# Performance work log

Hardware: AMD Instinct MI355X
Metric: run time of the kernel (lower is better)

Reference implementation:

```python
import jax, jax.numpy as jnp
import numpy as np
from jax import lax

N_SAMPLES = 64
POS_PER_BATCH = 16  # round(64 * 0.25)
POS_IOU = 0.5
EXCL_IOU = 0.1
IMG_H = 1024.0
IMG_W = 1024.0
BBOX_STD = jnp.array([0.1, 0.1, 0.2, 0.2], dtype=jnp.float32)
EPS = 1e-7


def _iou_matrix(rois, gts):
    # rois (R,4), gts (G,4) in (y1,x1,y2,x2) -> (R,G)
    y1 = jnp.maximum(rois[:, None, 0], gts[None, :, 0])
    x1 = jnp.maximum(rois[:, None, 1], gts[None, :, 1])
    y2 = jnp.minimum(rois[:, None, 2], gts[None, :, 2])
    x2 = jnp.minimum(rois[:, None, 3], gts[None, :, 3])
    inter = jnp.clip(y2 - y1, 0.0) * jnp.clip(x2 - x1, 0.0)
    area_r = jnp.clip(rois[:, 2] - rois[:, 0], 0.0) * jnp.clip(rois[:, 3] - rois[:, 1], 0.0)
    area_g = jnp.clip(gts[:, 2] - gts[:, 0], 0.0) * jnp.clip(gts[:, 3] - gts[:, 1], 0.0)
    union = area_r[:, None] + area_g[None, :] - inter
    return inter / jnp.maximum(union, EPS)


def _get_offsets(rois, gts):
    rh = jnp.maximum(rois[:, 2] - rois[:, 0], EPS)
    rw = jnp.maximum(rois[:, 3] - rois[:, 1], EPS)
    rcy = rois[:, 0] + 0.5 * rh
    rcx = rois[:, 1] + 0.5 * rw
    gh = jnp.maximum(gts[:, 2] - gts[:, 0], EPS)
    gw = jnp.maximum(gts[:, 3] - gts[:, 1], EPS)
    gcy = gts[:, 0] + 0.5 * gh
    gcx = gts[:, 1] + 0.5 * gw
    return jnp.stack([(gcy - rcy) / rh, (gcx - rcx) / rw,
                      jnp.log(gh / rh), jnp.log(gw / rw)], axis=-1)


def _per_image(roi, gt_bbox_n, gt_label):
    # roi (R,4) normalized; gt_bbox_n (G,4) normalized; gt_label (G,)
    roi_valid = jnp.any(roi != 0, axis=1)
    gt_valid = jnp.any(gt_bbox_n != 0, axis=1)
    ious = _iou_matrix(roi, gt_bbox_n)           # (R,G)
    ious = jnp.where(gt_valid[None, :], ious, -1.0)
    max_iou = ious.max(axis=1)
    idx_max_gt = ious.argmax(axis=1)

    pos = roi_valid & (max_iou >= POS_IOU)
    neg = roi_valid & (max_iou < POS_IOU) & (max_iou >= EXCL_IOU)
    R = roi.shape[0]
    ar = jnp.arange(R)
    # deterministic subsample (lowest index first) in place of tf.random_shuffle
    _, pos_idx = lax.top_k(jnp.where(pos, R - ar, 0), POS_PER_BATCH)
    _, neg_idx = lax.top_k(jnp.where(neg, R - ar, 0), N_SAMPLES)
    n_pos = jnp.minimum(pos.sum(), POS_PER_BATCH)
    n_neg = jnp.minimum(neg.sum(), N_SAMPLES - n_pos)

    slots = jnp.arange(N_SAMPLES)
    is_pos = slots < n_pos
    is_neg = (slots >= n_pos) & (slots < n_pos + n_neg)
    valid = is_pos | is_neg
    pidx = pos_idx[jnp.clip(slots, 0, POS_PER_BATCH - 1)]
    nidx = neg_idx[jnp.clip(slots - n_pos, 0, N_SAMPLES - 1)]
    ridx = jnp.where(is_pos, pidx, jnp.where(is_neg, nidx, 0))

    s_roi_raw = roi[ridx]                        # (64,4)
    gidx = idx_max_gt[ridx]
    s_gt = gt_bbox_n[gidx]
    vf = valid.astype(roi.dtype)[:, None]
    s_roi = s_roi_raw * vf
    s_off = (_get_offsets(s_roi_raw, s_gt) * vf) / BBOX_STD
    s_lab = jnp.where(is_pos, gt_label[gidx], 0).astype(jnp.int32)
    return s_roi, s_off, s_lab


def _forward(normalized_rois, gt_bboxes, gt_labels):
    gt_norm = gt_bboxes / jnp.array([IMG_H, IMG_W, IMG_H, IMG_W], dtype=gt_bboxes.dtype)
    return jax.vmap(_per_image)(normalized_rois, gt_norm, gt_labels)


def setup_inputs() -> dict:
    key = jax.random.key(0)
    k1, k2, k3, k4, k5, k6 = jax.random.split(key, 6)
    B, R, G = 8, 20000, 256
    cy = jax.random.uniform(k1, (B, G)) * IMG_H
    cx = jax.random.uniform(k2, (B, G)) * IMG_W
    sz = jax.random.uniform(k3, (B, G, 2)) * 180.0 + 20.0
    y1 = jnp.clip(cy - 0.5 * sz[..., 0], 0, IMG_H)
    y2 = jnp.clip(cy + 0.5 * sz[..., 0], 0, IMG_H)
    x1 = jnp.clip(cx - 0.5 * sz[..., 1], 0, IMG_W)
    x2 = jnp.clip(cx + 0.5 * sz[..., 1], 0, IMG_W)
    gt_bboxes = jnp.stack([y1, x1, y2, x2], axis=-1).astype(jnp.float32)
    gt_labels = jax.random.randint(k4, (B, G), 1, 81, dtype=jnp.int32)
    gt_norm = gt_bboxes / jnp.array([IMG_H, IMG_W, IMG_H, IMG_W], dtype=jnp.float32)
    # jittered copies of gt boxes guarantee positive RoIs
    jit = jnp.clip(jnp.tile(gt_norm, (1, 4, 1)) + 0.02 * jax.random.normal(k5, (B, 4 * G, 4)), 0.0, 1.0)
    rc = jax.random.uniform(k6, (B, R - 4 * G, 4))
    ry1 = jnp.minimum(rc[..., 0], rc[..., 2]); ry2 = jnp.maximum(rc[..., 0], rc[..., 2])
    rx1 = jnp.minimum(rc[..., 1], rc[..., 3]); rx2 = jnp.maximum(rc[..., 1], rc[..., 3])
    rand_rois = jnp.stack([ry1, rx1, ry2, rx2], axis=-1)
    normalized_rois = jnp.concatenate([jit, rand_rois], axis=1).astype(jnp.float32)
    return {"normalized_rois": normalized_rois, "gt_bboxes": gt_bboxes, "gt_labels": gt_labels}


def reference(normalized_rois, gt_bboxes, gt_labels):
    return _forward(normalized_rois, gt_bboxes, gt_labels)
```

## Files before the change

### kernel.cpp

```cpp
#include <hip/hip_runtime.h>

#pragma clang fp contract(off)

#define GMAX 256

__global__ __launch_bounds__(256) void iou_cls_kernel(
    const float* __restrict__ rois, const float* __restrict__ gts,
    int* __restrict__ cls_out, int R, int G)
{
    const int bi = blockIdx.y;
    const int r  = blockIdx.x * 256 + threadIdx.x;

    __shared__ float gy1[GMAX], gx1[GMAX], gy2[GMAX], gx2[GMAX], gar[GMAX];
    __shared__ int   gval[GMAX];

    const int t = threadIdx.x;
    if (t < G && t < GMAX) {
        const float4 g4 = *reinterpret_cast<const float4*>(gts + ((size_t)bi * G + t) * 4);
        const float s = 1.0f / 1024.0f;
        const float a = g4.x * s, b = g4.y * s, c = g4.z * s, d = g4.w * s;
        gy1[t] = a; gx1[t] = b; gy2[t] = c; gx2[t] = d;
        gval[t] = (a != 0.f) || (b != 0.f) || (c != 0.f) || (d != 0.f);
        gar[t] = fmaxf(c - a, 0.f) * fmaxf(d - b, 0.f);
    }
    __syncthreads();
    if (r >= R) return;

    const float4 rr = *reinterpret_cast<const float4*>(rois + ((size_t)bi * R + r) * 4);
    const bool rv = (rr.x != 0.f) || (rr.y != 0.f) || (rr.z != 0.f) || (rr.w != 0.f);
    const float ar = fmaxf(rr.z - rr.x, 0.f) * fmaxf(rr.w - rr.y, 0.f);

    float best = -1.0f;
    int   bidx = 0;
    #pragma unroll 4
    for (int g = 0; g < G; ++g) {
        const float y1 = fmaxf(rr.x, gy1[g]);
        const float x1 = fmaxf(rr.y, gx1[g]);
        const float y2 = fminf(rr.z, gy2[g]);
        const float x2 = fminf(rr.w, gx2[g]);
        const float inter = fmaxf(y2 - y1, 0.f) * fmaxf(x2 - x1, 0.f);
        const float uni   = (ar + gar[g]) - inter;
        float iou = inter / fmaxf(uni, 1e-7f);
        if (!gval[g]) iou = -1.0f;
        if (iou > best) { best = iou; bidx = g; }
    }

    const int pos = (rv && (best >= 0.5f)) ? 1 : 0;
    const int neg = (rv && (best < 0.5f) && (best >= 0.1f)) ? 1 : 0;
    cls_out[(size_t)bi * R + r] = (bidx & 0xFFFF) | (pos << 16) | (neg << 17);
}

__global__ __launch_bounds__(1024) void select_kernel(
    const float* __restrict__ rois, const float* __restrict__ gts,
    const int* __restrict__ labels, const int* __restrict__ cls,
    float* __restrict__ out, int R, int G, int B)
{
    const int bi  = blockIdx.x;
    const int tid = threadIdx.x;
    const int* clsb = cls + (size_t)bi * R;

    const int seg = (R + 1023) >> 10;
    const int s0 = tid * seg;
    const int s1 = min(R, s0 + seg);

    int pc = 0, nc = 0;
    for (int r = s0; r < s1; ++r) {
        const int c = clsb[r];
        pc += (c >> 16) & 1;
        nc += (c >> 17) & 1;
    }

    __shared__ int sp[1024], sn[1024];
    sp[tid] = pc; sn[tid] = nc;
    __syncthreads();
    for (int off = 1; off < 1024; off <<= 1) {
        const int vp = (tid >= off) ? sp[tid - off] : 0;
        const int vn = (tid >= off) ? sn[tid - off] : 0;
        __syncthreads();
        sp[tid] += vp; sn[tid] += vn;
        __syncthreads();
    }
    const int pbase = sp[tid] - pc;
    const int nbase = sn[tid] - nc;
    const int tot_p = sp[1023];
    const int tot_n = sn[1023];

    __shared__ int plist[16], nlist[64];
    if (tid < 16) plist[tid] = 0;
    if (tid < 64) nlist[tid] = 0;
    __syncthreads();

    if ((pbase < 16 && pc > 0) || (nbase < 64 && nc > 0)) {
        int p = pbase, n = nbase;
        for (int r = s0; r < s1; ++r) {
            const int c = clsb[r];
            if ((c >> 16) & 1) { if (p < 16) plist[p] = r; ++p; }
            if ((c >> 17) & 1) { if (n < 64) nlist[n] = r; ++n; }
        }
    }
    __syncthreads();

    const int n_pos = min(tot_p, 16);
    const int n_neg = min(tot_n, 64 - n_pos);

    if (tid < 64) {
        const int slot = tid;
        const bool isp = slot < n_pos;
        const bool isn = (!isp) && (slot < n_pos + n_neg);
        const int pidx = plist[min(slot, 15)];
        const int nidx = nlist[max(0, min(slot - n_pos, 63))];
        const int ridx = isp ? pidx : (isn ? nidx : 0);

        const float4 rr = *reinterpret_cast<const float4*>(rois + ((size_t)bi * R + ridx) * 4);
        const int gidx = clsb[ridx] & 0xFFFF;
        const float4 g4 = *reinterpret_cast<const float4*>(gts + ((size_t)bi * G + gidx) * 4);
        const float s = 1.0f / 1024.0f;
        const float g0 = g4.x * s, g1 = g4.y * s, g2 = g4.z * s, g3 = g4.w * s;

        const float vf = (isp || isn) ? 1.0f : 0.0f;
        const float eps = 1e-7f;

        const float rh  = fmaxf(rr.z - rr.x, eps);
        const float rw  = fmaxf(rr.w - rr.y, eps);
        const float rcy = rr.x + 0.5f * rh;
        const float rcx = rr.y + 0.5f * rw;
        const float gh  = fmaxf(g2 - g0, eps);
        const float gw  = fmaxf(g3 - g1, eps);
        const float gcy = g0 + 0.5f * gh;
        const float gcx = g1 + 0.5f * gw;

        float o0 = (gcy - rcy) / rh;
        float o1 = (gcx - rcx) / rw;
        float o2 = logf(gh / rh);
        float o3 = logf(gw / rw);
        o0 = (o0 * vf) / 0.1f;
        o1 = (o1 * vf) / 0.1f;
        o2 = (o2 * vf) / 0.2f;
        o3 = (o3 * vf) / 0.2f;

        const int base = bi * 64 + slot;
        float4* out_roi = reinterpret_cast<float4*>(out) + base;
        float4* out_off = reinterpret_cast<float4*>(out + (size_t)B * 256) + base;
        *out_roi = make_float4(rr.x * vf, rr.y * vf, rr.z * vf, rr.w * vf);
        *out_off = make_float4(o0, o1, o2, o3);

        const float lab = isp ? (float)labels[(size_t)bi * G + gidx] : 0.0f;
        out[(size_t)B * 512 + base] = lab;
    }
}

extern "C" void kernel_launch(void* const* d_in, const int* in_sizes, int n_in,
                              void* d_out, int out_size, void* d_ws, size_t ws_size,
                              hipStream_t stream)
{
    const float* rois   = (const float*)d_in[0];
    const float* gts    = (const float*)d_in[1];
    const int*   labels = (const int*)d_in[2];
    float* out = (float*)d_out;

    const int B = out_size / 576;
    const int G = in_sizes[2] / B;
    const int R = in_sizes[0] / (4 * B);

    int* cls = (int*)d_ws;

    dim3 gridA((R + 255) / 256, B);
    iou_cls_kernel<<<gridA, 256, 0, stream>>>(rois, gts, cls, R, G);
    select_kernel<<<B, 1024, 0, stream>>>(rois, gts, labels, cls, out, R, G, B);
}
```

Baseline: 111.2 us.

## Replace per-RoI class words with ballot bitmasks and recompute argmax only for selected slots

The first kernel now tracks only the max IoU, with no argmax. Invalid GTs are replaced by far-away boxes with zero area, which removes the per-iteration validity branch. Each wavefront packs its pos/neg flags into 64-bit ballot masks, cutting workspace writes and the select kernel's serial scan over R. The select kernel scans the popcounts with 512 threads, extracts indices with ffs, and recomputes argmax for only the 64 chosen RoIs, using 8 threads per slot combined with a 64-bit atomicMax key that keeps lowest-index tie-breaking. This adds a redundant IoU pass and assumes NW ≤ 512 and G ≤ 256.

```diff
diff --git a/kernel.cpp b/kernel.cpp
--- a/kernel.cpp
+++ b/kernel.cpp
@@ -3,103 +3,123 @@
 #pragma clang fp contract(off)
 
 #define GMAX 256
-
-__global__ __launch_bounds__(256) void iou_cls_kernel(
+#define K1B 128
+
+__device__ __forceinline__ unsigned int ordf(float f) {
+    unsigned int u = __float_as_uint(f);
+    return (u & 0x80000000u) ? ~u : (u | 0x80000000u);
+}
+
+__global__ __launch_bounds__(K1B) void iou_cls_kernel(
     const float* __restrict__ rois, const float* __restrict__ gts,
-    int* __restrict__ cls_out, int R, int G)
+    unsigned long long* __restrict__ pmask, unsigned long long* __restrict__ nmask,
+    int R, int G, int NW)
 {
     const int bi = blockIdx.y;
-    const int r  = blockIdx.x * 256 + threadIdx.x;
-
-    __shared__ float gy1[GMAX], gx1[GMAX], gy2[GMAX], gx2[GMAX], gar[GMAX];
-    __shared__ int   gval[GMAX];
-
-    const int t = threadIdx.x;
-    if (t < G && t < GMAX) {
+    const int r  = blockIdx.x * K1B + threadIdx.x;
+
+    __shared__ float4 gbox[GMAX];
+    __shared__ float  garea[GMAX];
+
+    for (int t = threadIdx.x; t < G; t += K1B) {
+        const float4 g4 = *reinterpret_cast<const float4*>(gts + ((size_t)bi * G + t) * 4);
+        const float s = 1.0f / 1024.0f;
+        float a = g4.x * s, b = g4.y * s, c = g4.z * s, d = g4.w * s;
+        const bool valid = (a != 0.f) || (b != 0.f) || (c != 0.f) || (d != 0.f);
+        if (!valid) { a = 4.f; b = 4.f; c = 4.f; d = 4.f; }
+        gbox[t]  = make_float4(a, b, c, d);
+        garea[t] = valid ? fmaxf(c - a, 0.f) * fmaxf(d - b, 0.f) : 0.0f;
+    }
+    __syncthreads();
+    if (r >= R) return;
+
+    const float4 rr = *reinterpret_cast<const float4*>(rois + ((size_t)bi * R + r) * 4);
+    const bool rv = (rr.x != 0.f) || (rr.y != 0.f) || (rr.z != 0.f) || (rr.w != 0.f);
+    const float ar = fmaxf(rr.z - rr.x, 0.f) * fmaxf(rr.w - rr.y, 0.f);
+
+    float best = 0.0f;
+    #pragma unroll 4
+    for (int g = 0; g < G; ++g) {
+        const float4 gb = gbox[g];
+        const float y1 = fmaxf(rr.x, gb.x);
+        const float x1 = fmaxf(rr.y, gb.y);
+        const float y2 = fminf(rr.z, gb.z);
+        const float x2 = fminf(rr.w, gb.w);
+        const float inter = fmaxf(y2 - y1, 0.f) * fmaxf(x2 - x1, 0.f);
+        const float uni   = (ar + garea[g]) - inter;
+        const float iou   = inter / fmaxf(uni, 1e-7f);
+        best = fmaxf(best, iou);
+    }
+
+    const bool pos = rv && (best >= 0.5f);
+    const bool neg = rv && !(best >= 0.5f) && (best >= 0.1f);
+
+    const unsigned long long bp = __ballot(pos);
+    const unsigned long long bn = __ballot(neg);
+    const int w = r >> 6;
+    if ((threadIdx.x & 63) == 0 && w < NW) {
+        pmask[(size_t)bi * NW + w] = bp;
+        nmask[(size_t)bi * NW + w] = bn;
+    }
+}
+
+__global__ __launch_bounds__(512) void select_kernel(
+    const float* __restrict__ rois, const float* __restrict__ gts,
+    const int* __restrict__ labels,
+    const unsigned long long* __restrict__ pmask, const unsigned long long* __restrict__ nmask,
+    float* __restrict__ out, int R, int G, int B, int NW)
+{
+    const int bi  = blockIdx.x;
+    const int tid = threadIdx.x;
+
+    __shared__ int sp[512], sn[512];
+    __shared__ float4 sgt[GMAX];
+    __shared__ float  sgv[GMAX];
+    __shared__ int plist[16], nlist[64];
+    __shared__ int sridx[64];
+    __shared__ unsigned long long skey[64];
+
+    for (int t = tid; t < G; t += 512) {
         const float4 g4 = *reinterpret_cast<const float4*>(gts + ((size_t)bi * G + t) * 4);
         const float s = 1.0f / 1024.0f;
         const float a = g4.x * s, b = g4.y * s, c = g4.z * s, d = g4.w * s;
-        gy1[t] = a; gx1[t] = b; gy2[t] = c; gx2[t] = d;
-        gval[t] = (a != 0.f) || (b != 0.f) || (c != 0.f) || (d != 0.f);
-        gar[t] = fmaxf(c - a, 0.f) * fmaxf(d - b, 0.f);
-    }
-    __syncthreads();
-    if (r >= R) return;
-
-    const float4 rr = *reinterpret_cast<const float4*>(rois + ((size_t)bi * R + r) * 4);
-    const bool rv = (rr.x != 0.f) || (rr.y != 0.f) || (rr.z != 0.f) || (rr.w != 0.f);
-    const float ar = fmaxf(rr.z - rr.x, 0.f) * fmaxf(rr.w - rr.y, 0.f);
-
-    float best = -1.0f;
-    int   bidx = 0;
-    #pragma unroll 4
-    for (int g = 0; g < G; ++g) {
-        const float y1 = fmaxf(rr.x, gy1[g]);
-        const float x1 = fmaxf(rr.y, gx1[g]);
-        const float y2 = fminf(rr.z, gy2[g]);
-        const float x2 = fminf(rr.w, gx2[g]);
-        const float inter = fmaxf(y2 - y1, 0.f) * fmaxf(x2 - x1, 0.f);
-        const float uni   = (ar + gar[g]) - inter;
-        float iou = inter / fmaxf(uni, 1e-7f);
-        if (!gval[g]) iou = -1.0f;
-        if (iou > best) { best = iou; bidx = g; }
-    }
-
-    const int pos = (rv && (best >= 0.5f)) ? 1 : 0;
-    const int neg = (rv && (best < 0.5f) && (best >= 0.1f)) ? 1 : 0;
-    cls_out[(size_t)bi * R + r] = (bidx & 0xFFFF) | (pos << 16) | (neg << 17);
-}
-
-__global__ __launch_bounds__(1024) void select_kernel(
-    const float* __restrict__ rois, const float* __restrict__ gts,
-    const int* __restrict__ labels, const int* __restrict__ cls,
-    float* __restrict__ out, int R, int G, int B)
-{
-    const int bi  = blockIdx.x;
-    const int tid = threadIdx.x;
-    const int* clsb = cls + (size_t)bi * R;
-
-    const int seg = (R + 1023) >> 10;
-    const int s0 = tid * seg;
-    const int s1 = min(R, s0 + seg);
-
-    int pc = 0, nc = 0;
-    for (int r = s0; r < s1; ++r) {
-        const int c = clsb[r];
-        pc += (c >> 16) & 1;
-        nc += (c >> 17) & 1;
-    }
-
-    __shared__ int sp[1024], sn[1024];
-    sp[tid] = pc; sn[tid] = nc;
-    __syncthreads();
-    for (int off = 1; off < 1024; off <<= 1) {
+        sgt[t] = make_float4(a, b, c, d);
+        sgv[t] = ((a != 0.f) || (b != 0.f) || (c != 0.f) || (d != 0.f)) ? 1.0f : 0.0f;
+    }
+
+    unsigned long long mp = 0ull, mn = 0ull;
+    if (tid < NW) {
+        mp = pmask[(size_t)bi * NW + tid];
+        mn = nmask[(size_t)bi * NW + tid];
+    }
+    const int cp = __popcll(mp);
+    const int cn = __popcll(mn);
+    sp[tid] = cp; sn[tid] = cn;
+    if (tid < 16) plist[tid] = 0;
+    if (tid < 64) nlist[tid] = 0;
+    __syncthreads();
+    for (int off = 1; off < 512; off <<= 1) {
         const int vp = (tid >= off) ? sp[tid - off] : 0;
         const int vn = (tid >= off) ? sn[tid - off] : 0;
         __syncthreads();
         sp[tid] += vp; sn[tid] += vn;
         __syncthreads();
     }
-    const int pbase = sp[tid] - pc;
-    const int nbase = sn[tid] - nc;
-    const int tot_p = sp[1023];
-    const int tot_n = sn[1023];
-
-    __shared__ int plist[16], nlist[64];
-    if (tid < 16) plist[tid] = 0;
-    if (tid < 64) nlist[tid] = 0;
-    __syncthreads();
-
-    if ((pbase < 16 && pc > 0) || (nbase < 64 && nc > 0)) {
-        int p = pbase, n = nbase;
-        for (int r = s0; r < s1; ++r) {
-            const int c = clsb[r];
-            if ((c >> 16) & 1) { if (p < 16) plist[p] = r; ++p; }
-            if ((c >> 17) & 1) { if (n < 64) nlist[n] = r; ++n; }
-        }
-    }
-    __syncthreads();
-
+    const int basep = sp[tid] - cp;
+    const int basen = sn[tid] - cn;
+
+    if (mp && basep < 16) {
+        int rank = basep; unsigned long long m = mp;
+        while (m && rank < 16) { const int b = __ffsll(m) - 1; plist[rank++] = tid * 64 + b; m &= m - 1; }
+    }
+    if (mn && basen < 64) {
+        int rank = basen; unsigned long long m = mn;
+        while (m && rank < 64) { const int b = __ffsll(m) - 1; nlist[rank++] = tid * 64 + b; m &= m - 1; }
+    }
+    __syncthreads();
+
+    const int tot_p = sp[511];
+    const int tot_n = sn[511];
     const int n_pos = min(tot_p, 16);
     const int n_neg = min(tot_n, 64 - n_pos);
 
@@ -107,16 +127,49 @@
         const int slot = tid;
         const bool isp = slot < n_pos;
         const bool isn = (!isp) && (slot < n_pos + n_neg);
-        const int pidx = plist[min(slot, 15)];
-        const int nidx = nlist[max(0, min(slot - n_pos, 63))];
-        const int ridx = isp ? pidx : (isn ? nidx : 0);
-
+        sridx[slot] = isp ? plist[slot] : (isn ? nlist[slot - n_pos] : 0);
+        skey[slot]  = 0ull;
+    }
+    __syncthreads();
+
+    {
+        const int slot = tid >> 3;
+        const int sub  = tid & 7;
+        const int ridx = sridx[slot];
         const float4 rr = *reinterpret_cast<const float4*>(rois + ((size_t)bi * R + ridx) * 4);
-        const int gidx = clsb[ridx] & 0xFFFF;
-        const float4 g4 = *reinterpret_cast<const float4*>(gts + ((size_t)bi * G + gidx) * 4);
-        const float s = 1.0f / 1024.0f;
-        const float g0 = g4.x * s, g1 = g4.y * s, g2 = g4.z * s, g3 = g4.w * s;
-
+        const float ar = fmaxf(rr.z - rr.x, 0.f) * fmaxf(rr.w - rr.y, 0.f);
+        float best = -1.0f;
+        int bidx = sub * 32;
+        for (int j = 0; j < 32; ++j) {
+            const int g = sub * 32 + j;
+            if (g >= G) break;
+            const float4 gb = sgt[g];
+            const float y1 = fmaxf(rr.x, gb.x);
+            const float x1 = fmaxf(rr.y, gb.y);
+            const float y2 = fminf(rr.z, gb.z);
+            const float x2 = fminf(rr.w, gb.w);
+            const float inter = fmaxf(y2 - y1, 0.f) * fmaxf(x2 - x1, 0.f);
+            const float ga = fmaxf(gb.z - gb.x, 0.f) * fmaxf(gb.w - gb.y, 0.f);
+            const float uni = (ar + ga) - inter;
+            float v = inter / fmaxf(uni, 1e-7f);
+            if (sgv[g] == 0.0f) v = -1.0f;
+            if (v > best) { best = v; bidx = g; }
+        }
+        const unsigned long long key =
+            ((unsigned long long)ordf(best) << 32) | (unsigned int)(~(unsigned int)bidx);
+        atomicMax(&skey[slot], key);
+    }
+    __syncthreads();
+
+    if (tid < 64) {
+        const int slot = tid;
+        const bool isp = slot < n_pos;
+        const bool isn = (!isp) && (slot < n_pos + n_neg);
+        const int ridx = sridx[slot];
+        const int gidx = (int)(~(unsigned int)(skey[slot] & 0xFFFFFFFFull));
+
+        const float4 rr = *reinterpret_cast<const float4*>(rois + ((size_t)bi * R + ridx) * 4);
+        const float4 gb = sgt[gidx];
         const float vf = (isp || isn) ? 1.0f : 0.0f;
         const float eps = 1e-7f;
 
@@ -124,10 +177,10 @@
         const float rw  = fmaxf(rr.w - rr.y, eps);
         const float rcy = rr.x + 0.5f * rh;
         const float rcx = rr.y + 0.5f * rw;
-        const float gh  = fmaxf(g2 - g0, eps);
-        const float gw  = fmaxf(g3 - g1, eps);
-        const float gcy = g0 + 0.5f * gh;
-        const float gcx = g1 + 0.5f * gw;
+        const float gh  = fmaxf(gb.z - gb.x, eps);
+        const float gw  = fmaxf(gb.w - gb.y, eps);
+        const float gcy = gb.x + 0.5f * gh;
+        const float gcx = gb.y + 0.5f * gw;
 
         float o0 = (gcy - rcy) / rh;
         float o1 = (gcx - rcx) / rw;
@@ -139,13 +192,9 @@
         o3 = (o3 * vf) / 0.2f;
 
         const int base = bi * 64 + slot;
-        float4* out_roi = reinterpret_cast<float4*>(out) + base;
-        float4* out_off = reinterpret_cast<float4*>(out + (size_t)B * 256) + base;
-        *out_roi = make_float4(rr.x * vf, rr.y * vf, rr.z * vf, rr.w * vf);
-        *out_off = make_float4(o0, o1, o2, o3);
-
-        const float lab = isp ? (float)labels[(size_t)bi * G + gidx] : 0.0f;
-        out[(size_t)B * 512 + base] = lab;
+        reinterpret_cast<float4*>(out)[base] = make_float4(rr.x * vf, rr.y * vf, rr.z * vf, rr.w * vf);
+        reinterpret_cast<float4*>(out + (size_t)B * 256)[base] = make_float4(o0, o1, o2, o3);
+        out[(size_t)B * 512 + base] = isp ? (float)labels[(size_t)bi * G + gidx] : 0.0f;
     }
 }
 
@@ -161,10 +210,12 @@
     const int B = out_size / 576;
     const int G = in_sizes[2] / B;
     const int R = in_sizes[0] / (4 * B);
-
-    int* cls = (int*)d_ws;
-
-    dim3 gridA((R + 255) / 256, B);
-    iou_cls_kernel<<<gridA, 256, 0, stream>>>(rois, gts, cls, R, G);
-    select_kernel<<<B, 1024, 0, stream>>>(rois, gts, labels, cls, out, R, G, B);
-}
+    const int NW = (R + 63) / 64;
+
+    unsigned long long* pmask = (unsigned long long*)d_ws;
+    unsigned long long* nmask = pmask + (size_t)B * NW;
+
+    dim3 gridA((R + K1B - 1) / K1B, B);
+    iou_cls_kernel<<<gridA, K1B, 0, stream>>>(rois, gts, pmask, nmask, R, G, NW);
+    select_kernel<<<B, 512, 0, stream>>>(rois, gts, labels, pmask, nmask, out, R, G, B, NW);
+}
```

Result: slower. 121.9 us (+9.6%).
